# Optimization experiments

Measured on AMD Instinct MI355X. Metric: run time of the kernel, lower is better.

## Reference

```python
import jax, jax.numpy as jnp
import numpy as np


def setup_inputs() -> dict:
    key = jax.random.key(0)
    k1, k2 = jax.random.split(key)
    B, C, h, w = 8, 128, 56, 56
    query_feature = jax.random.normal(k1, (B, C, h, w), dtype=jnp.float32)
    support_feature = jax.random.normal(k2, (B, C, h, w), dtype=jnp.float32)
    return {"query_feature": query_feature, "support_feature": support_feature}


def reference(query_feature, support_feature):
    q, s = query_feature, support_feature
    B, C, h, w = support_feature.shape
    N = h * w
    # torch .view semantics == row-major reshape (NOT a transpose)
    qf = jnp.reshape(query_feature, (B, N, C))      # [B, N, C]
    sf = jnp.reshape(support_feature, (B, C, N))    # [B, C, N]
    batch_adj = jnp.einsum('bnc,bcm->bnm', qf, sf)  # [B, N, N]
    attn = jax.nn.softmax(batch_adj, axis=-1)
    query_logits = jnp.einsum('bnm,bmc->bnc', attn, qf)          # [B, N, C]
    attention_mask = jax.nn.sigmoid(jnp.sum(batch_adj, axis=-1)) # [B, N]
    query_logits = query_logits * attention_mask[..., None]
    sf2 = jnp.reshape(support_feature, (B, N, C))   # another raw view
    support_logits = sf2 * attention_mask[..., None]
    query_logits = jnp.reshape(query_logits, (B, C, h, w))
    support_logits = jnp.reshape(support_logits, (B, C, h, w))
    return (q + query_logits, s + support_logits)
```

## Files before the change

### kernel.cpp

```cpp
#include <hip/hip_runtime.h>
#include <math.h>

#define B_ 8
#define C_ 128
#define N_ 3136
#define MT 64
#define QTBIG 128
#define TILES 49
#define QTILES 25

typedef short bf16x8 __attribute__((ext_vector_type(8)));
typedef float f32x4 __attribute__((ext_vector_type(4)));

__device__ __forceinline__ unsigned short f2bf(float f) {
    union { float f; unsigned u; } x; x.f = f;
    return (unsigned short)((x.u + 0x8000u) >> 16);
}

__device__ __forceinline__ void gl_lds16(const void* g, void* l) {
    __builtin_amdgcn_global_load_lds(
        (const __attribute__((address_space(1))) unsigned int*)g,
        (__attribute__((address_space(3))) unsigned int*)l, 16, 0, 0);
}

__global__ __launch_bounds__(256) void colsum_kernel(const float* __restrict__ s,
                                                     float* __restrict__ csum) {
    int blk = blockIdx.x;
    const float* p = s + (size_t)blk * N_;
    float acc = 0.f;
    for (int i = threadIdx.x; i < N_; i += 256) acc += p[i];
#pragma unroll
    for (int off = 32; off > 0; off >>= 1) acc += __shfl_down(acc, off, 64);
    __shared__ float part[4];
    if ((threadIdx.x & 63) == 0) part[threadIdx.x >> 6] = acc;
    __syncthreads();
    if (threadIdx.x == 0) csum[blk] = part[0] + part[1] + part[2] + part[3];
}

__global__ __launch_bounds__(256) void prep_kernel(const float* __restrict__ q,
                                                   const float* __restrict__ s,
                                                   unsigned short* __restrict__ sfT,
                                                   unsigned short* __restrict__ qfT,
                                                   float* __restrict__ csum) {
    __shared__ unsigned short T[8448];
    const int tid = threadIdx.x, bid = blockIdx.x;
    const int b = bid & 7, m0 = (bid >> 3) * 64;
    const float* sb = s + (size_t)b * C_ * N_;
    const float* qb = q + (size_t)b * C_ * N_;

    unsigned short (*TA)[132] = (unsigned short (*)[132])T;
#pragma unroll
    for (int st = 0; st < 8; ++st) {
        int idx = st * 256 + tid;
        int c = idx >> 4, m4 = (idx & 15) * 4;
        float4 v = *(const float4*)&sb[(size_t)c * N_ + m0 + m4];
        TA[m4 + 0][c] = f2bf(v.x);
        TA[m4 + 1][c] = f2bf(v.y);
        TA[m4 + 2][c] = f2bf(v.z);
        TA[m4 + 3][c] = f2bf(v.w);
        float part = v.x + v.y + v.z + v.w;
        part += __shfl_xor(part, 1, 64);
        part += __shfl_xor(part, 2, 64);
        part += __shfl_xor(part, 4, 64);
        part += __shfl_xor(part, 8, 64);
        if ((tid & 15) == 0) atomicAdd(&csum[b * C_ + c], part);
    }
    __syncthreads();
    {
        unsigned short* dst = sfT + (size_t)b * N_ * C_;
#pragma unroll
        for (int st = 0; st < 4; ++st) {
            int g = st * 256 + tid;
            int mr = g >> 4, p = g & 15;
            int lch = p ^ (mr & 15);
            const unsigned short* src = &TA[mr][lch * 8];
            ushort4 a = *(const ushort4*)src;
            ushort4 bq = *(const ushort4*)(src + 4);
            uint4 w;
            w.x = a.x | ((unsigned)a.y << 16);   w.y = a.z | ((unsigned)a.w << 16);
            w.z = bq.x | ((unsigned)bq.y << 16); w.w = bq.z | ((unsigned)bq.w << 16);
            *(uint4*)&dst[(size_t)(m0 + mr) * C_ + p * 8] = w;
        }
    }
    __syncthreads();

    unsigned short (*TB)[66] = (unsigned short (*)[66])T;
#pragma unroll
    for (int st = 0; st < 8; ++st) {
        int idx = st * 256 + tid;
        int r = idx >> 5, c4 = (idx & 31) * 4;
        float4 v = *(const float4*)&qb[(size_t)(m0 + r) * C_ + c4];
        TB[c4 + 0][r] = f2bf(v.x);
        TB[c4 + 1][r] = f2bf(v.y);
        TB[c4 + 2][r] = f2bf(v.z);
        TB[c4 + 3][r] = f2bf(v.w);
    }
    __syncthreads();
    {
        unsigned short* dst = qfT + (size_t)b * C_ * N_;
#pragma unroll
        for (int st = 0; st < 4; ++st) {
            int g = st * 256 + tid;
            int c = g >> 3, p = g & 7;
            int lch = p ^ (c & 7);
            const unsigned short* src = &TB[c][lch * 8];
            ushort2 a0 = *(const ushort2*)(src);
            ushort2 a1 = *(const ushort2*)(src + 2);
            ushort2 a2 = *(const ushort2*)(src + 4);
            ushort2 a3 = *(const ushort2*)(src + 6);
            uint4 w;
            w.x = a0.x | ((unsigned)a0.y << 16); w.y = a1.x | ((unsigned)a1.y << 16);
            w.z = a2.x | ((unsigned)a2.y << 16); w.w = a3.x | ((unsigned)a3.y << 16);
            *(uint4*)&dst[(size_t)c * N_ + m0 + p * 8] = w;
        }
    }
}

__global__ __launch_bounds__(256, 2) void fused_mfma_kernel(
    const float* __restrict__ q, const float* __restrict__ s,
    const float* __restrict__ csum, const unsigned short* __restrict__ sfT,
    const unsigned short* __restrict__ qfT,
    float* __restrict__ out0, float* __restrict__ out1) {

    __shared__ __align__(16) unsigned short Kb[2][MT * C_];
    __shared__ __align__(16) unsigned short Vb[2][C_ * MT];
    __shared__ float csum_l[C_];
    __shared__ float mask_l[QTBIG];

    const int tid = threadIdx.x;
    const int lane = tid & 63;
    const int wave = tid >> 6;
    const int l15 = lane & 15;
    const int quad = lane >> 4;
    const int bid = blockIdx.x;
    const int b = bid & 7;
    const int n0 = (bid >> 3) * QTBIG;

    const float* qb = q + (size_t)b * C_ * N_;
    const float* sb = s + (size_t)b * C_ * N_;
    const unsigned short* sfTb = sfT + (size_t)b * N_ * C_;
    const unsigned short* qfTb = qfT + (size_t)b * C_ * N_;

    const int sig_base = ((l15 >> 2) << 3) + (l15 & 3);

#pragma unroll
    for (int st = 0; st < 4; ++st) {
        int i = st * 256 + tid;
        gl_lds16(sfTb + (size_t)(i >> 4) * C_ + (i & 15) * 8,
                 &Kb[0][(st * 256 + wave * 64) * 8]);
        gl_lds16(qfTb + (size_t)(i >> 3) * N_ + (i & 7) * 8,
                 &Vb[0][(st * 256 + wave * 64) * 8]);
    }
    if (tid < C_) csum_l[tid] = csum[b * C_ + tid];

    bf16x8 qa[2][4];
#pragma unroll
    for (int rt = 0; rt < 2; ++rt) {
        int grow = n0 + wave * 32 + rt * 16 + l15;
        if (grow > N_ - 1) grow = N_ - 1;
#pragma unroll
        for (int ks = 0; ks < 4; ++ks) {
            int c0 = ks * 32 + quad * 8;
            float4 f0 = *(const float4*)&qb[(size_t)grow * C_ + c0];
            float4 f1 = *(const float4*)&qb[(size_t)grow * C_ + c0 + 4];
            union { unsigned short u[8]; bf16x8 v; } t;
            t.u[0] = f2bf(f0.x); t.u[1] = f2bf(f0.y);
            t.u[2] = f2bf(f0.z); t.u[3] = f2bf(f0.w);
            t.u[4] = f2bf(f1.x); t.u[5] = f2bf(f1.y);
            t.u[6] = f2bf(f1.z); t.u[7] = f2bf(f1.w);
            qa[rt][ks] = t.v;
        }
    }
    __syncthreads();

    {
        int row_l = tid >> 1, half = tid & 1;
        int grow = n0 + row_l; if (grow > N_ - 1) grow = N_ - 1;
        const float* qr = &qb[(size_t)grow * C_ + half * 64];
        const float* cs = &csum_l[half * 64];
        float d = 0.f;
#pragma unroll 4
        for (int c = 0; c < 64; c += 4) {
            float4 v = *(const float4*)&qr[c];
            d += v.x * cs[c] + v.y * cs[c + 1] + v.z * cs[c + 2] + v.w * cs[c + 3];
        }
        d += __shfl_xor(d, 1, 64);
        if (half == 0) mask_l[row_l] = 1.0f / (1.0f + __expf(-d));
    }

    f32x4 O[2][8];
#pragma unroll
    for (int rt = 0; rt < 2; ++rt)
#pragma unroll
        for (int nt = 0; nt < 8; ++nt) O[rt][nt] = (f32x4){0.f, 0.f, 0.f, 0.f};
    float dsum[2] = {0.f, 0.f};

    for (int t = 0; t < TILES; ++t) {
        const int cur = t & 1;
        __syncthreads();

        if (t + 1 < TILES) {
            const int nxt = cur ^ 1;
            const size_t m1 = (size_t)(t + 1) * MT;
#pragma unroll
            for (int st = 0; st < 4; ++st) {
                int i = st * 256 + tid;
                gl_lds16(sfTb + (m1 + (i >> 4)) * C_ + (i & 15) * 8,
                         &Kb[nxt][(st * 256 + wave * 64) * 8]);
                gl_lds16(qfTb + (size_t)(i >> 3) * N_ + m1 + (i & 7) * 8,
                         &Vb[nxt][(st * 256 + wave * 64) * 8]);
            }
        }

        f32x4 acc[4][2];
#pragma unroll
        for (int ct = 0; ct < 4; ++ct) {
            acc[ct][0] = (f32x4){0.f, 0.f, 0.f, 0.f};
            acc[ct][1] = (f32x4){0.f, 0.f, 0.f, 0.f};
            const int mrow = sig_base + ((ct & 1) << 2) + ((ct >> 1) << 5);
#pragma unroll
            for (int ks = 0; ks < 4; ++ks) {
                int ch = (ks * 4 + quad) ^ (mrow & 15);
                bf16x8 af = *(const bf16x8*)&Kb[cur][mrow * C_ + ch * 8];
                acc[ct][0] = __builtin_amdgcn_mfma_f32_16x16x32_bf16(af, qa[0][ks], acc[ct][0], 0, 0, 0);
                acc[ct][1] = __builtin_amdgcn_mfma_f32_16x16x32_bf16(af, qa[1][ks], acc[ct][1], 0, 0, 0);
            }
        }

        bf16x8 pa[2][2];
#pragma unroll
        for (int k2 = 0; k2 < 2; ++k2)
#pragma unroll
            for (int rt = 0; rt < 2; ++rt) {
                float e0 = __expf(acc[2 * k2 + 0][rt][0]);
                float e1 = __expf(acc[2 * k2 + 0][rt][1]);
                float e2 = __expf(acc[2 * k2 + 0][rt][2]);
                float e3 = __expf(acc[2 * k2 + 0][rt][3]);
                float e4 = __expf(acc[2 * k2 + 1][rt][0]);
                float e5 = __expf(acc[2 * k2 + 1][rt][1]);
                float e6 = __expf(acc[2 * k2 + 1][rt][2]);
                float e7 = __expf(acc[2 * k2 + 1][rt][3]);
                dsum[rt] += ((e0 + e1) + (e2 + e3)) + ((e4 + e5) + (e6 + e7));
                union { unsigned short u[8]; bf16x8 v; } pk;
                pk.u[0] = f2bf(e0); pk.u[1] = f2bf(e1);
                pk.u[2] = f2bf(e2); pk.u[3] = f2bf(e3);
                pk.u[4] = f2bf(e4); pk.u[5] = f2bf(e5);
                pk.u[6] = f2bf(e6); pk.u[7] = f2bf(e7);
                pa[rt][k2] = pk.v;
            }

#pragma unroll
        for (int k2 = 0; k2 < 2; ++k2)
#pragma unroll
            for (int nt = 0; nt < 8; ++nt) {
                const int crow = nt * 16 + l15;
                int ch = (k2 * 4 + quad) ^ (crow & 7);
                bf16x8 vf = *(const bf16x8*)&Vb[cur][crow * MT + ch * 8];
                O[0][nt] = __builtin_amdgcn_mfma_f32_16x16x32_bf16(pa[0][k2], vf, O[0][nt], 0, 0, 0);
                O[1][nt] = __builtin_amdgcn_mfma_f32_16x16x32_bf16(pa[1][k2], vf, O[1][nt], 0, 0, 0);
            }
    }

#pragma unroll
    for (int rt = 0; rt < 2; ++rt) {
        float d = dsum[rt];
        d += __shfl_xor(d, 16, 64);
        d += __shfl_xor(d, 32, 64);
        dsum[rt] = d;
    }

    const size_t bo = (size_t)b * C_ * N_;
#pragma unroll
    for (int rt = 0; rt < 2; ++rt)
#pragma unroll
        for (int r = 0; r < 4; ++r) {
            int row_l = wave * 32 + rt * 16 + quad * 4 + r;
            int grow = n0 + row_l;
            float denom = __shfl(dsum[rt], quad * 4 + r, 64);
            if (grow < N_) {
                float scl = mask_l[row_l] / denom;
#pragma unroll
                for (int nt = 0; nt < 8; ++nt) {
                    int col = nt * 16 + l15;
                    out0[bo + (size_t)grow * C_ + col] =
                        qb[(size_t)grow * C_ + col] + O[rt][nt][r] * scl;
                }
            }
        }
#pragma unroll
    for (int i = 0; i < 16; ++i) {
        int idx = i * 256 + tid;
        int row_l = idx >> 5, c4 = (idx & 31) * 4;
        int grow = n0 + row_l;
        if (grow < N_) {
            float4 sv = *(const float4*)&sb[(size_t)grow * C_ + c4];
            float om = 1.0f + mask_l[row_l];
            float4 o;
            o.x = sv.x * om; o.y = sv.y * om; o.z = sv.z * om; o.w = sv.w * om;
            *(float4*)&out1[bo + (size_t)grow * C_ + c4] = o;
        }
    }
}

__global__ __launch_bounds__(256, 2) void fused_kernel(const float* __restrict__ q,
                                                       const float* __restrict__ s,
                                                       const float* __restrict__ csum,
                                                       float* __restrict__ out0,
                                                       float* __restrict__ out1) {
    __shared__ float QtT[C_][68];
    __shared__ float Kt[C_ * 32];
    __shared__ float Vt[32 * C_];
    __shared__ float PT[32][68];
    __shared__ float mask_l[64];
    __shared__ float csum_l[C_];

    const int t = threadIdx.x;
    const int l = t & 63, w = t >> 6, tx = t & 15, ty = t >> 4;
    const int bid = blockIdx.x, b = bid & 7, n0 = (bid >> 3) * 64;
    const float* qb = q + (size_t)b * C_ * N_;
    const float* sb = s + (size_t)b * C_ * N_;

#pragma unroll
    for (int jj = 0; jj < 2; ++jj) {
        int c = l + 64 * jj;
#pragma unroll
        for (int i = 0; i < 16; ++i) QtT[c][w + 4 * i] = qb[(size_t)(n0 + w + 4 * i) * C_ + c];
    }
    if (t < C_) csum_l[t] = csum[b * C_ + t];
    __syncthreads();
    if (t < 64) {
        float d = 0.f;
        for (int c = 0; c < C_; ++c) d += QtT[c][t] * csum_l[c];
        mask_l[t] = 1.0f / (1.0f + __expf(-d));
    }
    float4 Oa[4], Ob[4];
#pragma unroll
    for (int i = 0; i < 4; ++i) { Oa[i] = make_float4(0,0,0,0); Ob[i] = make_float4(0,0,0,0); }
    float m_r[4], l_r[4];
#pragma unroll
    for (int i = 0; i < 4; ++i) { m_r[i] = -3.0e38f; l_r[i] = 0.f; }

    for (int mt = 0; mt < N_ / 32; ++mt) {
        const int m0 = mt * 32;
        __syncthreads();
#pragma unroll
        for (int i = 0; i < 4; ++i) {
            int s4 = (w * 4 + i) * 64 + l;
            int c = s4 >> 3, mq = (s4 & 7) * 4;
            *(float4*)&Kt[c * 32 + mq] = *(const float4*)&sb[(size_t)c * N_ + m0 + mq];
            *(float4*)&Vt[s4 * 4] = *(const float4*)&qb[(size_t)m0 * C_ + s4 * 4];
        }
        __syncthreads();
        float a[4][2];
#pragma unroll
        for (int i = 0; i < 4; ++i) a[i][0] = a[i][1] = 0.f;
#pragma unroll 4
        for (int k = 0; k < C_; ++k) {
            const float4 qv = *(const float4*)&QtT[k][4 * ty];
            const float2 kv = *(const float2*)&Kt[k * 32 + 2 * tx];
            a[0][0] = fmaf(qv.x, kv.x, a[0][0]); a[0][1] = fmaf(qv.x, kv.y, a[0][1]);
            a[1][0] = fmaf(qv.y, kv.x, a[1][0]); a[1][1] = fmaf(qv.y, kv.y, a[1][1]);
            a[2][0] = fmaf(qv.z, kv.x, a[2][0]); a[2][1] = fmaf(qv.z, kv.y, a[2][1]);
            a[3][0] = fmaf(qv.w, kv.x, a[3][0]); a[3][1] = fmaf(qv.w, kv.y, a[3][1]);
        }
#pragma unroll
        for (int i = 0; i < 4; ++i) {
            float tm = fmaxf(a[i][0], a[i][1]);
            tm = fmaxf(tm, __shfl_xor(tm, 1, 64)); tm = fmaxf(tm, __shfl_xor(tm, 2, 64));
            tm = fmaxf(tm, __shfl_xor(tm, 4, 64)); tm = fmaxf(tm, __shfl_xor(tm, 8, 64));
            float nm = fmaxf(m_r[i], tm);
            float al = __expf(m_r[i] - nm);
            m_r[i] = nm;
            float p0 = __expf(a[i][0] - nm), p1 = __expf(a[i][1] - nm);
            float ts = p0 + p1;
            ts += __shfl_xor(ts, 1, 64); ts += __shfl_xor(ts, 2, 64);
            ts += __shfl_xor(ts, 4, 64); ts += __shfl_xor(ts, 8, 64);
            l_r[i] = l_r[i] * al + ts;
            PT[2 * tx + 0][4 * ty + i] = p0;
            PT[2 * tx + 1][4 * ty + i] = p1;
            Oa[i].x *= al; Oa[i].y *= al; Oa[i].z *= al; Oa[i].w *= al;
            Ob[i].x *= al; Ob[i].y *= al; Ob[i].z *= al; Ob[i].w *= al;
        }
        __syncthreads();
#pragma unroll 2
        for (int j = 0; j < 32; ++j) {
            const float4 pv = *(const float4*)&PT[j][4 * ty];
            const float4 v0 = *(const float4*)&Vt[j * C_ + 4 * tx];
            const float4 v1 = *(const float4*)&Vt[j * C_ + 4 * tx + 64];
            Oa[0].x = fmaf(pv.x, v0.x, Oa[0].x); Oa[0].y = fmaf(pv.x, v0.y, Oa[0].y);
            Oa[0].z = fmaf(pv.x, v0.z, Oa[0].z); Oa[0].w = fmaf(pv.x, v0.w, Oa[0].w);
            Ob[0].x = fmaf(pv.x, v1.x, Ob[0].x); Ob[0].y = fmaf(pv.x, v1.y, Ob[0].y);
            Ob[0].z = fmaf(pv.x, v1.z, Ob[0].z); Ob[0].w = fmaf(pv.x, v1.w, Ob[0].w);
            Oa[1].x = fmaf(pv.y, v0.x, Oa[1].x); Oa[1].y = fmaf(pv.y, v0.y, Oa[1].y);
            Oa[1].z = fmaf(pv.y, v0.z, Oa[1].z); Oa[1].w = fmaf(pv.y, v0.w, Oa[1].w);
            Ob[1].x = fmaf(pv.y, v1.x, Ob[1].x); Ob[1].y = fmaf(pv.y, v1.y, Ob[1].y);
            Ob[1].z = fmaf(pv.y, v1.z, Ob[1].z); Ob[1].w = fmaf(pv.y, v1.w, Ob[1].w);
            Oa[2].x = fmaf(pv.z, v0.x, Oa[2].x); Oa[2].y = fmaf(pv.z, v0.y, Oa[2].y);
            Oa[2].z = fmaf(pv.z, v0.z, Oa[2].z); Oa[2].w = fmaf(pv.z, v0.w, Oa[2].w);
            Ob[2].x = fmaf(pv.z, v1.x, Ob[2].x); Ob[2].y = fmaf(pv.z, v1.y, Ob[2].y);
            Ob[2].z = fmaf(pv.z, v1.z, Ob[2].z); Ob[2].w = fmaf(pv.z, v1.w, Ob[2].w);
            Oa[3].x = fmaf(pv.w, v0.x, Oa[3].x); Oa[3].y = fmaf(pv.w, v0.y, Oa[3].y);
            Oa[3].z = fmaf(pv.w, v0.z, Oa[3].z); Oa[3].w = fmaf(pv.w, v0.w, Oa[3].w);
            Ob[3].x = fmaf(pv.w, v1.x, Ob[3].x); Ob[3].y = fmaf(pv.w, v1.y, Ob[3].y);
            Ob[3].z = fmaf(pv.w, v1.z, Ob[3].z); Ob[3].w = fmaf(pv.w, v1.w, Ob[3].w);
        }
    }
#pragma unroll
    for (int i = 0; i < 4; ++i) {
        const int r = 4 * ty + i;
        const float mk = mask_l[r];
        const float scl = mk / l_r[i];
        const float om = 1.0f + mk;
        const size_t row = (size_t)b * C_ * N_ + (size_t)(n0 + r) * C_;
#pragma unroll
        for (int h = 0; h < 2; ++h) {
            const int c = 4 * tx + 64 * h;
            const float4 ov = h ? Ob[i] : Oa[i];
            float4 qv = *(const float4*)&qb[(size_t)(n0 + r) * C_ + c];
            float4 sv = *(const float4*)&sb[(size_t)(n0 + r) * C_ + c];
            float4 o0, o1;
            o0.x = qv.x + ov.x * scl; o0.y = qv.y + ov.y * scl;
            o0.z = qv.z + ov.z * scl; o0.w = qv.w + ov.w * scl;
            o1.x = sv.x * om; o1.y = sv.y * om; o1.z = sv.z * om; o1.w = sv.w * om;
            *(float4*)&out0[row + c] = o0;
            *(float4*)&out1[row + c] = o1;
        }
    }
}

extern "C" void kernel_launch(void* const* d_in, const int* in_sizes, int n_in,
                              void* d_out, int out_size, void* d_ws, size_t ws_size,
                              hipStream_t stream) {
    const float* q = (const float*)d_in[0];
    const float* s = (const float*)d_in[1];
    float* out0 = (float*)d_out;
    float* out1 = out0 + (size_t)B_ * C_ * N_;
    float* csum = (float*)d_ws;

    const size_t bf16_elems = (size_t)B_ * N_ * C_;
    const size_t need = 4096 + 2 * bf16_elems * sizeof(unsigned short);

    if (ws_size >= need) {
        unsigned short* sfT = (unsigned short*)((char*)d_ws + 4096);
        unsigned short* qfT = sfT + bf16_elems;
        hipMemsetAsync(csum, 0, B_ * C_ * sizeof(float), stream);
        prep_kernel<<<B_ * TILES, 256, 0, stream>>>(q, s, sfT, qfT, csum);
        fused_mfma_kernel<<<B_ * QTILES, 256, 0, stream>>>(q, s, csum, sfT, qfT, out0, out1);
    } else {
        colsum_kernel<<<B_ * C_, 256, 0, stream>>>(s, csum);
        fused_kernel<<<B_ * (N_ / 64), 256, 0, stream>>>(q, s, csum, out0, out1);
    }
}
```

Baseline: 180.8 us.

## Split key range across two blocks and add separate combine kernel

The attention kernel now splits the key tiles into two halves handled by separate blocks, doubling the grid to improve CU occupancy. Each block writes unnormalized partial outputs and row sums to workspace, and a new combine kernel sums them, computes the sigmoid mask, and writes both outputs. The column sum moves from atomics in the prep kernel to the standalone colsum kernel. This adds fp32 partial-output traffic, an extra launch, and a larger workspace requirement.

Measured after the change: 149.0 us. -17.6%, faster.

```diff
diff --git a/kernel.cpp b/kernel.cpp
--- a/kernel.cpp
+++ b/kernel.cpp
@@ -8,6 +8,7 @@
 #define QTBIG 128
 #define TILES 49
 #define QTILES 25
+#define SPLIT0 25
 
 typedef short bf16x8 __attribute__((ext_vector_type(8)));
 typedef float f32x4 __attribute__((ext_vector_type(4)));
@@ -40,8 +41,7 @@
 __global__ __launch_bounds__(256) void prep_kernel(const float* __restrict__ q,
                                                    const float* __restrict__ s,
                                                    unsigned short* __restrict__ sfT,
-                                                   unsigned short* __restrict__ qfT,
-                                                   float* __restrict__ csum) {
+                                                   unsigned short* __restrict__ qfT) {
     __shared__ unsigned short T[8448];
     const int tid = threadIdx.x, bid = blockIdx.x;
     const int b = bid & 7, m0 = (bid >> 3) * 64;
@@ -58,12 +58,6 @@
         TA[m4 + 1][c] = f2bf(v.y);
         TA[m4 + 2][c] = f2bf(v.z);
         TA[m4 + 3][c] = f2bf(v.w);
-        float part = v.x + v.y + v.z + v.w;
-        part += __shfl_xor(part, 1, 64);
-        part += __shfl_xor(part, 2, 64);
-        part += __shfl_xor(part, 4, 64);
-        part += __shfl_xor(part, 8, 64);
-        if ((tid & 15) == 0) atomicAdd(&csum[b * C_ + c], part);
     }
     __syncthreads();
     {
@@ -116,16 +110,14 @@
     }
 }
 
-__global__ __launch_bounds__(256, 2) void fused_mfma_kernel(
-    const float* __restrict__ q, const float* __restrict__ s,
-    const float* __restrict__ csum, const unsigned short* __restrict__ sfT,
+__global__ __launch_bounds__(256, 2) void fused_split_kernel(
+    const float* __restrict__ q,
+    const unsigned short* __restrict__ sfT,
     const unsigned short* __restrict__ qfT,
-    float* __restrict__ out0, float* __restrict__ out1) {
+    float* __restrict__ Opart, float* __restrict__ dpart) {
 
     __shared__ __align__(16) unsigned short Kb[2][MT * C_];
     __shared__ __align__(16) unsigned short Vb[2][C_ * MT];
-    __shared__ float csum_l[C_];
-    __shared__ float mask_l[QTBIG];
 
     const int tid = threadIdx.x;
     const int lane = tid & 63;
@@ -134,24 +126,30 @@
     const int quad = lane >> 4;
     const int bid = blockIdx.x;
     const int b = bid & 7;
-    const int n0 = (bid >> 3) * QTBIG;
+    const int rest = bid >> 3;
+    const int qt = rest % QTILES;
+    const int split = rest / QTILES;
+    const int n0 = qt * QTBIG;
+    const int t0 = split ? SPLIT0 : 0;
+    const int t1 = split ? TILES : SPLIT0;
 
     const float* qb = q + (size_t)b * C_ * N_;
-    const float* sb = s + (size_t)b * C_ * N_;
     const unsigned short* sfTb = sfT + (size_t)b * N_ * C_;
     const unsigned short* qfTb = qfT + (size_t)b * C_ * N_;
 
     const int sig_base = ((l15 >> 2) << 3) + (l15 & 3);
 
-#pragma unroll
-    for (int st = 0; st < 4; ++st) {
-        int i = st * 256 + tid;
-        gl_lds16(sfTb + (size_t)(i >> 4) * C_ + (i & 15) * 8,
-                 &Kb[0][(st * 256 + wave * 64) * 8]);
-        gl_lds16(qfTb + (size_t)(i >> 3) * N_ + (i & 7) * 8,
-                 &Vb[0][(st * 256 + wave * 64) * 8]);
-    }
-    if (tid < C_) csum_l[tid] = csum[b * C_ + tid];
+    {
+        const size_t m1 = (size_t)t0 * MT;
+#pragma unroll
+        for (int st = 0; st < 4; ++st) {
+            int i = st * 256 + tid;
+            gl_lds16(sfTb + (m1 + (i >> 4)) * C_ + (i & 15) * 8,
+                     &Kb[0][(st * 256 + wave * 64) * 8]);
+            gl_lds16(qfTb + (size_t)(i >> 3) * N_ + m1 + (i & 7) * 8,
+                     &Vb[0][(st * 256 + wave * 64) * 8]);
+        }
+    }
 
     bf16x8 qa[2][4];
 #pragma unroll
@@ -171,22 +169,6 @@
             qa[rt][ks] = t.v;
         }
     }
-    __syncthreads();
-
-    {
-        int row_l = tid >> 1, half = tid & 1;
-        int grow = n0 + row_l; if (grow > N_ - 1) grow = N_ - 1;
-        const float* qr = &qb[(size_t)grow * C_ + half * 64];
-        const float* cs = &csum_l[half * 64];
-        float d = 0.f;
-#pragma unroll 4
-        for (int c = 0; c < 64; c += 4) {
-            float4 v = *(const float4*)&qr[c];
-            d += v.x * cs[c] + v.y * cs[c + 1] + v.z * cs[c + 2] + v.w * cs[c + 3];
-        }
-        d += __shfl_xor(d, 1, 64);
-        if (half == 0) mask_l[row_l] = 1.0f / (1.0f + __expf(-d));
-    }
 
     f32x4 O[2][8];
 #pragma unroll
@@ -195,13 +177,14 @@
         for (int nt = 0; nt < 8; ++nt) O[rt][nt] = (f32x4){0.f, 0.f, 0.f, 0.f};
     float dsum[2] = {0.f, 0.f};
 
-    for (int t = 0; t < TILES; ++t) {
-        const int cur = t & 1;
+    const int ntiles = t1 - t0;
+    for (int tt = 0; tt < ntiles; ++tt) {
+        const int cur = tt & 1;
         __syncthreads();
 
-        if (t + 1 < TILES) {
+        if (tt + 1 < ntiles) {
             const int nxt = cur ^ 1;
-            const size_t m1 = (size_t)(t + 1) * MT;
+            const size_t m1 = (size_t)(t0 + tt + 1) * MT;
 #pragma unroll
             for (int st = 0; st < 4; ++st) {
                 int i = st * 256 + tid;
@@ -266,39 +249,81 @@
         float d = dsum[rt];
         d += __shfl_xor(d, 16, 64);
         d += __shfl_xor(d, 32, 64);
-        dsum[rt] = d;
-    }
-
-    const size_t bo = (size_t)b * C_ * N_;
+        if (quad == 0) {
+            int grow = n0 + wave * 32 + rt * 16 + l15;
+            if (grow < N_)
+                dpart[(size_t)(split * 8 + b) * N_ + grow] = d;
+        }
+    }
+
 #pragma unroll
     for (int rt = 0; rt < 2; ++rt)
 #pragma unroll
         for (int r = 0; r < 4; ++r) {
-            int row_l = wave * 32 + rt * 16 + quad * 4 + r;
-            int grow = n0 + row_l;
-            float denom = __shfl(dsum[rt], quad * 4 + r, 64);
+            int grow = n0 + wave * 32 + rt * 16 + quad * 4 + r;
             if (grow < N_) {
-                float scl = mask_l[row_l] / denom;
-#pragma unroll
-                for (int nt = 0; nt < 8; ++nt) {
-                    int col = nt * 16 + l15;
-                    out0[bo + (size_t)grow * C_ + col] =
-                        qb[(size_t)grow * C_ + col] + O[rt][nt][r] * scl;
-                }
+                float* dst = Opart + ((size_t)(split * 8 + b) * N_ + grow) * C_;
+#pragma unroll
+                for (int nt = 0; nt < 8; ++nt)
+                    dst[nt * 16 + l15] = O[rt][nt][r];
             }
         }
-#pragma unroll
-    for (int i = 0; i < 16; ++i) {
-        int idx = i * 256 + tid;
-        int row_l = idx >> 5, c4 = (idx & 31) * 4;
-        int grow = n0 + row_l;
-        if (grow < N_) {
-            float4 sv = *(const float4*)&sb[(size_t)grow * C_ + c4];
-            float om = 1.0f + mask_l[row_l];
-            float4 o;
-            o.x = sv.x * om; o.y = sv.y * om; o.z = sv.z * om; o.w = sv.w * om;
-            *(float4*)&out1[bo + (size_t)grow * C_ + c4] = o;
-        }
+}
+
+__global__ __launch_bounds__(256) void combine_kernel(
+    const float* __restrict__ q, const float* __restrict__ s,
+    const float* __restrict__ csum, const float* __restrict__ Opart,
+    const float* __restrict__ dpart,
+    float* __restrict__ out0, float* __restrict__ out1) {
+
+    __shared__ float cs[C_];
+    const int tid = threadIdx.x, bid = blockIdx.x;
+    const int b = bid & 7, r0 = (bid >> 3) * 32;
+    if (tid < C_) cs[tid] = csum[b * C_ + tid];
+    __syncthreads();
+
+    const int lane = tid & 63, wave = tid >> 6;
+    const int row_l = wave * 8 + (lane >> 3);
+    const int j = lane & 7;
+    const int grow = r0 + row_l;
+    const size_t base = (size_t)b * N_ * C_ + (size_t)grow * C_;
+
+    float4 qv[4];
+    float dot = 0.f;
+#pragma unroll
+    for (int k = 0; k < 4; ++k) {
+        int c = k * 32 + j * 4;
+        qv[k] = *(const float4*)&q[base + c];
+        dot += qv[k].x * cs[c] + qv[k].y * cs[c + 1] +
+               qv[k].z * cs[c + 2] + qv[k].w * cs[c + 3];
+    }
+    dot += __shfl_xor(dot, 1, 64);
+    dot += __shfl_xor(dot, 2, 64);
+    dot += __shfl_xor(dot, 4, 64);
+    const float mask = 1.0f / (1.0f + __expf(-dot));
+
+    const float dtot = dpart[(size_t)b * N_ + grow] +
+                       dpart[(size_t)(8 + b) * N_ + grow];
+    const float scl = mask / dtot;
+    const float om = 1.0f + mask;
+
+    const size_t p0 = ((size_t)b * N_ + grow) * C_;
+    const size_t p1 = p0 + (size_t)8 * N_ * C_;
+#pragma unroll
+    for (int k = 0; k < 4; ++k) {
+        int c = k * 32 + j * 4;
+        float4 oa = *(const float4*)&Opart[p0 + c];
+        float4 ob = *(const float4*)&Opart[p1 + c];
+        float4 sv = *(const float4*)&s[base + c];
+        float4 r0v, r1v;
+        r0v.x = qv[k].x + (oa.x + ob.x) * scl;
+        r0v.y = qv[k].y + (oa.y + ob.y) * scl;
+        r0v.z = qv[k].z + (oa.z + ob.z) * scl;
+        r0v.w = qv[k].w + (oa.w + ob.w) * scl;
+        r1v.x = sv.x * om; r1v.y = sv.y * om;
+        r1v.z = sv.z * om; r1v.w = sv.w * om;
+        *(float4*)&out0[base + c] = r0v;
+        *(float4*)&out1[base + c] = r1v;
     }
 }
 
@@ -437,17 +462,22 @@
     float* out1 = out0 + (size_t)B_ * C_ * N_;
     float* csum = (float*)d_ws;
 
-    const size_t bf16_elems = (size_t)B_ * N_ * C_;
-    const size_t need = 4096 + 2 * bf16_elems * sizeof(unsigned short);
-
+    const size_t elems = (size_t)B_ * N_ * C_;
+    const size_t need = 4096
+                      + 2 * elems * sizeof(unsigned short)
+                      + 2 * elems * sizeof(float)
+                      + 2 * (size_t)B_ * N_ * sizeof(float);
+
+    colsum_kernel<<<B_ * C_, 256, 0, stream>>>(s, csum);
     if (ws_size >= need) {
         unsigned short* sfT = (unsigned short*)((char*)d_ws + 4096);
-        unsigned short* qfT = sfT + bf16_elems;
-        hipMemsetAsync(csum, 0, B_ * C_ * sizeof(float), stream);
-        prep_kernel<<<B_ * TILES, 256, 0, stream>>>(q, s, sfT, qfT, csum);
-        fused_mfma_kernel<<<B_ * QTILES, 256, 0, stream>>>(q, s, csum, sfT, qfT, out0, out1);
+        unsigned short* qfT = sfT + elems;
+        float* Opart = (float*)(qfT + elems);
+        float* dpart = Opart + 2 * elems;
+        prep_kernel<<<B_ * TILES, 256, 0, stream>>>(q, s, sfT, qfT);
+        fused_split_kernel<<<2 * QTILES * B_, 256, 0, stream>>>(q, sfT, qfT, Opart, dpart);
+        combine_kernel<<<B_ * (N_ / 32), 256, 0, stream>>>(q, s, csum, Opart, dpart, out0, out1);
     } else {
-        colsum_kernel<<<B_ * C_, 256, 0, stream>>>(s, csum);
         fused_kernel<<<B_ * (N_ / 64), 256, 0, stream>>>(q, s, csum, out0, out1);
     }
 }
```

## Split key dimension across two blocks with atomic-counter last-block combine

Applied to the files above, without the earlier changes.

The fused attention kernel now splits the 3136 key positions into two halves, one per block, which doubles the grid from 200 to 400 blocks so more of the CUs are busy. Each block writes its partial O and softmax denominators to workspace and bumps an atomic counter. The second block to arrive merges both halves, computes the sigmoid mask and writes the outputs. The key tile is halved to 32, with a matching change to the prep kernel's V layout, and launch bounds now allow 3 blocks per CU. The cost is extra global traffic for the partial results, plus a counter that is never reset and relies on parity across calls.

After: 231.9 us. 1.28x slower.

```diff
diff --git a/kernel.cpp b/kernel.cpp
--- a/kernel.cpp
+++ b/kernel.cpp
@@ -4,10 +4,12 @@
 #define B_ 8
 #define C_ 128
 #define N_ 3136
-#define MT 64
+#define MT 32
 #define QTBIG 128
-#define TILES 49
+#define TILES32 98
+#define SPLIT_T 49
 #define QTILES 25
+#define PTILES 49
 
 typedef short bf16x8 __attribute__((ext_vector_type(8)));
 typedef float f32x4 __attribute__((ext_vector_type(4)));
@@ -101,9 +103,10 @@
 #pragma unroll
         for (int st = 0; st < 4; ++st) {
             int g = st * 256 + tid;
-            int c = g >> 3, p = g & 7;
-            int lch = p ^ (c & 7);
-            const unsigned short* src = &TB[c][lch * 8];
+            int c = g >> 3, pp = g & 7;
+            int grp = pp >> 2, p = pp & 3;
+            int lch = p ^ (c & 3);
+            const unsigned short* src = &TB[c][grp * 32 + lch * 8];
             ushort2 a0 = *(const ushort2*)(src);
             ushort2 a1 = *(const ushort2*)(src + 2);
             ushort2 a2 = *(const ushort2*)(src + 4);
@@ -111,21 +114,23 @@
             uint4 w;
             w.x = a0.x | ((unsigned)a0.y << 16); w.y = a1.x | ((unsigned)a1.y << 16);
             w.z = a2.x | ((unsigned)a2.y << 16); w.w = a3.x | ((unsigned)a3.y << 16);
-            *(uint4*)&dst[(size_t)c * N_ + m0 + p * 8] = w;
-        }
-    }
-}
-
-__global__ __launch_bounds__(256, 2) void fused_mfma_kernel(
+            *(uint4*)&dst[(size_t)c * N_ + m0 + grp * 32 + p * 8] = w;
+        }
+    }
+}
+
+__global__ __launch_bounds__(256, 3) void fused_split_kernel(
     const float* __restrict__ q, const float* __restrict__ s,
-    const float* __restrict__ csum, const unsigned short* __restrict__ sfT,
+    const float* __restrict__ csum,
+    const unsigned short* __restrict__ sfT,
     const unsigned short* __restrict__ qfT,
+    float* __restrict__ Opart, float* __restrict__ dpart,
+    int* __restrict__ cnt,
     float* __restrict__ out0, float* __restrict__ out1) {
 
     __shared__ __align__(16) unsigned short Kb[2][MT * C_];
     __shared__ __align__(16) unsigned short Vb[2][C_ * MT];
-    __shared__ float csum_l[C_];
-    __shared__ float mask_l[QTBIG];
+    __shared__ int flag_s;
 
     const int tid = threadIdx.x;
     const int lane = tid & 63;
@@ -134,7 +139,11 @@
     const int quad = lane >> 4;
     const int bid = blockIdx.x;
     const int b = bid & 7;
-    const int n0 = (bid >> 3) * QTBIG;
+    const int rest = bid >> 3;
+    const int qt = rest % QTILES;
+    const int split = rest / QTILES;
+    const int n0 = qt * QTBIG;
+    const int t0 = split * SPLIT_T;
 
     const float* qb = q + (size_t)b * C_ * N_;
     const float* sb = s + (size_t)b * C_ * N_;
@@ -143,15 +152,17 @@
 
     const int sig_base = ((l15 >> 2) << 3) + (l15 & 3);
 
-#pragma unroll
-    for (int st = 0; st < 4; ++st) {
-        int i = st * 256 + tid;
-        gl_lds16(sfTb + (size_t)(i >> 4) * C_ + (i & 15) * 8,
-                 &Kb[0][(st * 256 + wave * 64) * 8]);
-        gl_lds16(qfTb + (size_t)(i >> 3) * N_ + (i & 7) * 8,
-                 &Vb[0][(st * 256 + wave * 64) * 8]);
-    }
-    if (tid < C_) csum_l[tid] = csum[b * C_ + tid];
+    {
+        const size_t m1 = (size_t)t0 * MT;
+#pragma unroll
+        for (int j = 0; j < 2; ++j) {
+            int i = j * 256 + tid;
+            gl_lds16(sfTb + (m1 + (i >> 4)) * C_ + (i & 15) * 8,
+                     &Kb[0][(j * 256 + wave * 64) * 8]);
+            gl_lds16(qfTb + (size_t)(i >> 2) * N_ + m1 + (i & 3) * 8,
+                     &Vb[0][(j * 256 + wave * 64) * 8]);
+        }
+    }
 
     bf16x8 qa[2][4];
 #pragma unroll
@@ -171,22 +182,6 @@
             qa[rt][ks] = t.v;
         }
     }
-    __syncthreads();
-
-    {
-        int row_l = tid >> 1, half = tid & 1;
-        int grow = n0 + row_l; if (grow > N_ - 1) grow = N_ - 1;
-        const float* qr = &qb[(size_t)grow * C_ + half * 64];
-        const float* cs = &csum_l[half * 64];
-        float d = 0.f;
-#pragma unroll 4
-        for (int c = 0; c < 64; c += 4) {
-            float4 v = *(const float4*)&qr[c];
-            d += v.x * cs[c] + v.y * cs[c + 1] + v.z * cs[c + 2] + v.w * cs[c + 3];
-        }
-        d += __shfl_xor(d, 1, 64);
-        if (half == 0) mask_l[row_l] = 1.0f / (1.0f + __expf(-d));
-    }
 
     f32x4 O[2][8];
 #pragma unroll
@@ -195,29 +190,29 @@
         for (int nt = 0; nt < 8; ++nt) O[rt][nt] = (f32x4){0.f, 0.f, 0.f, 0.f};
     float dsum[2] = {0.f, 0.f};
 
-    for (int t = 0; t < TILES; ++t) {
-        const int cur = t & 1;
+    for (int tt = 0; tt < SPLIT_T; ++tt) {
+        const int cur = tt & 1;
         __syncthreads();
 
-        if (t + 1 < TILES) {
+        if (tt + 1 < SPLIT_T) {
             const int nxt = cur ^ 1;
-            const size_t m1 = (size_t)(t + 1) * MT;
-#pragma unroll
-            for (int st = 0; st < 4; ++st) {
-                int i = st * 256 + tid;
+            const size_t m1 = (size_t)(t0 + tt + 1) * MT;
+#pragma unroll
+            for (int j = 0; j < 2; ++j) {
+                int i = j * 256 + tid;
                 gl_lds16(sfTb + (m1 + (i >> 4)) * C_ + (i & 15) * 8,
-                         &Kb[nxt][(st * 256 + wave * 64) * 8]);
-                gl_lds16(qfTb + (size_t)(i >> 3) * N_ + m1 + (i & 7) * 8,
-                         &Vb[nxt][(st * 256 + wave * 64) * 8]);
+                         &Kb[nxt][(j * 256 + wave * 64) * 8]);
+                gl_lds16(qfTb + (size_t)(i >> 2) * N_ + m1 + (i & 3) * 8,
+                         &Vb[nxt][(j * 256 + wave * 64) * 8]);
             }
         }
 
-        f32x4 acc[4][2];
-#pragma unroll
-        for (int ct = 0; ct < 4; ++ct) {
+        f32x4 acc[2][2];
+#pragma unroll
+        for (int ct = 0; ct < 2; ++ct) {
             acc[ct][0] = (f32x4){0.f, 0.f, 0.f, 0.f};
             acc[ct][1] = (f32x4){0.f, 0.f, 0.f, 0.f};
-            const int mrow = sig_base + ((ct & 1) << 2) + ((ct >> 1) << 5);
+            const int mrow = sig_base + ct * 4;
 #pragma unroll
             for (int ks = 0; ks < 4; ++ks) {
                 int ch = (ks * 4 + quad) ^ (mrow & 15);
@@ -227,38 +222,31 @@
             }
         }
 
-        bf16x8 pa[2][2];
-#pragma unroll
-        for (int k2 = 0; k2 < 2; ++k2)
-#pragma unroll
-            for (int rt = 0; rt < 2; ++rt) {
-                float e0 = __expf(acc[2 * k2 + 0][rt][0]);
-                float e1 = __expf(acc[2 * k2 + 0][rt][1]);
-                float e2 = __expf(acc[2 * k2 + 0][rt][2]);
-                float e3 = __expf(acc[2 * k2 + 0][rt][3]);
-                float e4 = __expf(acc[2 * k2 + 1][rt][0]);
-                float e5 = __expf(acc[2 * k2 + 1][rt][1]);
-                float e6 = __expf(acc[2 * k2 + 1][rt][2]);
-                float e7 = __expf(acc[2 * k2 + 1][rt][3]);
-                dsum[rt] += ((e0 + e1) + (e2 + e3)) + ((e4 + e5) + (e6 + e7));
-                union { unsigned short u[8]; bf16x8 v; } pk;
-                pk.u[0] = f2bf(e0); pk.u[1] = f2bf(e1);
-                pk.u[2] = f2bf(e2); pk.u[3] = f2bf(e3);
-                pk.u[4] = f2bf(e4); pk.u[5] = f2bf(e5);
-                pk.u[6] = f2bf(e6); pk.u[7] = f2bf(e7);
-                pa[rt][k2] = pk.v;
-            }
-
-#pragma unroll
-        for (int k2 = 0; k2 < 2; ++k2)
-#pragma unroll
-            for (int nt = 0; nt < 8; ++nt) {
-                const int crow = nt * 16 + l15;
-                int ch = (k2 * 4 + quad) ^ (crow & 7);
-                bf16x8 vf = *(const bf16x8*)&Vb[cur][crow * MT + ch * 8];
-                O[0][nt] = __builtin_amdgcn_mfma_f32_16x16x32_bf16(pa[0][k2], vf, O[0][nt], 0, 0, 0);
-                O[1][nt] = __builtin_amdgcn_mfma_f32_16x16x32_bf16(pa[1][k2], vf, O[1][nt], 0, 0, 0);
-            }
+        bf16x8 pa[2];
+#pragma unroll
+        for (int rt = 0; rt < 2; ++rt) {
+            union { unsigned short u[8]; bf16x8 v; } pk;
+            float da = 0.f;
+#pragma unroll
+            for (int ct = 0; ct < 2; ++ct)
+#pragma unroll
+                for (int r = 0; r < 4; ++r) {
+                    float e = __expf(acc[ct][rt][r]);
+                    da += e;
+                    pk.u[ct * 4 + r] = f2bf(e);
+                }
+            dsum[rt] += da;
+            pa[rt] = pk.v;
+        }
+
+#pragma unroll
+        for (int nt = 0; nt < 8; ++nt) {
+            const int crow = nt * 16 + l15;
+            int ch = quad ^ (crow & 3);
+            bf16x8 vf = *(const bf16x8*)&Vb[cur][crow * MT + ch * 8];
+            O[0][nt] = __builtin_amdgcn_mfma_f32_16x16x32_bf16(pa[0], vf, O[0][nt], 0, 0, 0);
+            O[1][nt] = __builtin_amdgcn_mfma_f32_16x16x32_bf16(pa[1], vf, O[1][nt], 0, 0, 0);
+        }
     }
 
 #pragma unroll
@@ -267,26 +255,77 @@
         d += __shfl_xor(d, 16, 64);
         d += __shfl_xor(d, 32, 64);
         dsum[rt] = d;
-    }
-
+        if (quad == 0) {
+            int grow = n0 + wave * 32 + rt * 16 + l15;
+            if (grow < N_)
+                dpart[(size_t)(split * 8 + b) * N_ + grow] = d;
+        }
+    }
+
+#pragma unroll
+    for (int rt = 0; rt < 2; ++rt)
+#pragma unroll
+        for (int r = 0; r < 4; ++r) {
+            int grow = n0 + wave * 32 + rt * 16 + quad * 4 + r;
+            if (grow < N_) {
+                float* dst = Opart + ((size_t)(split * 8 + b) * N_ + grow) * C_;
+#pragma unroll
+                for (int nt = 0; nt < 8; ++nt)
+                    dst[nt * 16 + l15] = O[rt][nt][r];
+            }
+        }
+
+    __threadfence();
+    __syncthreads();
+    if (tid == 0) flag_s = atomicAdd(&cnt[b * QTILES + qt], 1);
+    __syncthreads();
+    if ((flag_s & 1) == 0) return;
+    __threadfence();
+
+    float* cs = (float*)&Kb[0][0];
+    float* mask_l = cs + C_;
+    if (tid < C_) cs[tid] = csum[b * C_ + tid];
+    __syncthreads();
+
+    const int other = split ^ 1;
+    const float* OthO = Opart + (size_t)(other * 8 + b) * N_ * C_;
+    const float* Othd = dpart + (size_t)(other * 8 + b) * N_;
     const size_t bo = (size_t)b * C_ * N_;
+
 #pragma unroll
     for (int rt = 0; rt < 2; ++rt)
 #pragma unroll
         for (int r = 0; r < 4; ++r) {
             int row_l = wave * 32 + rt * 16 + quad * 4 + r;
             int grow = n0 + row_l;
-            float denom = __shfl(dsum[rt], quad * 4 + r, 64);
+            float myd = __shfl(dsum[rt], quad * 4 + r, 64);
             if (grow < N_) {
-                float scl = mask_l[row_l] / denom;
+                float othd = Othd[grow];
+                float qv[8];
+                float dotp = 0.f;
 #pragma unroll
                 for (int nt = 0; nt < 8; ++nt) {
                     int col = nt * 16 + l15;
-                    out0[bo + (size_t)grow * C_ + col] =
-                        qb[(size_t)grow * C_ + col] + O[rt][nt][r] * scl;
+                    qv[nt] = qb[(size_t)grow * C_ + col];
+                    dotp += qv[nt] * cs[col];
+                }
+                dotp += __shfl_xor(dotp, 1, 64);
+                dotp += __shfl_xor(dotp, 2, 64);
+                dotp += __shfl_xor(dotp, 4, 64);
+                dotp += __shfl_xor(dotp, 8, 64);
+                float mask = 1.0f / (1.0f + __expf(-dotp));
+                if (l15 == 0) mask_l[row_l] = mask;
+                float scl = mask / (myd + othd);
+#pragma unroll
+                for (int nt = 0; nt < 8; ++nt) {
+                    int col = nt * 16 + l15;
+                    float tot = O[rt][nt][r] + OthO[(size_t)grow * C_ + col];
+                    out0[bo + (size_t)grow * C_ + col] = qv[nt] + tot * scl;
                 }
             }
         }
+    __syncthreads();
+
 #pragma unroll
     for (int i = 0; i < 16; ++i) {
         int idx = i * 256 + tid;
@@ -437,15 +476,23 @@
     float* out1 = out0 + (size_t)B_ * C_ * N_;
     float* csum = (float*)d_ws;
 
-    const size_t bf16_elems = (size_t)B_ * N_ * C_;
-    const size_t need = 4096 + 2 * bf16_elems * sizeof(unsigned short);
+    const size_t elems = (size_t)B_ * N_ * C_;
+    const size_t need = 4096
+                      + 2 * elems * sizeof(unsigned short)
+                      + 2 * elems * sizeof(float)
+                      + 2 * (size_t)B_ * N_ * sizeof(float)
+                      + (size_t)B_ * QTILES * sizeof(int);
 
     if (ws_size >= need) {
         unsigned short* sfT = (unsigned short*)((char*)d_ws + 4096);
-        unsigned short* qfT = sfT + bf16_elems;
+        unsigned short* qfT = sfT + elems;
+        float* Opart = (float*)(qfT + elems);
+        float* dpart = Opart + 2 * elems;
+        int* cnt = (int*)(dpart + 2 * (size_t)B_ * N_);
         hipMemsetAsync(csum, 0, B_ * C_ * sizeof(float), stream);
-        prep_kernel<<<B_ * TILES, 256, 0, stream>>>(q, s, sfT, qfT, csum);
-        fused_mfma_kernel<<<B_ * QTILES, 256, 0, stream>>>(q, s, csum, sfT, qfT, out0, out1);
+        prep_kernel<<<B_ * PTILES, 256, 0, stream>>>(q, s, sfT, qfT, csum);
+        fused_split_kernel<<<2 * QTILES * B_, 256, 0, stream>>>(q, s, csum, sfT, qfT,
+                                                                Opart, dpart, cnt, out0, out1);
     } else {
         colsum_kernel<<<B_ * C_, 256, 0, stream>>>(s, csum);
         fused_kernel<<<B_ * (N_ / 64), 256, 0, stream>>>(q, s, csum, out0, out1);
```

## Split key dimension across four blocks with atomic partial reduction

Applied to the files above, without the earlier changes.

The fused attention kernel now splits the 49 key tiles of each query tile across four blocks, so the launch grows from 200 to 800 workgroups and fills more CUs. Each split adds its unnormalised output and row denominators into global fp32 buffers with atomics, and a counter picks the last block to finish, which computes the mask and writes both outputs. This works because softmax does no max subtraction, so partial sums add directly. The cost is an extra memset of a large fp32 buffer, heavy global atomic traffic (about 400K atomics per split pass), and a reread of the partial sums.

Result: slower. 234.5 us (+29.7%).

```diff
diff --git a/kernel.cpp b/kernel.cpp
--- a/kernel.cpp
+++ b/kernel.cpp
@@ -8,6 +8,7 @@
 #define QTBIG 128
 #define TILES 49
 #define QTILES 25
+#define NSPLIT 4
 
 typedef short bf16x8 __attribute__((ext_vector_type(8)));
 typedef float f32x4 __attribute__((ext_vector_type(4)));
@@ -116,16 +117,18 @@
     }
 }
 
-__global__ __launch_bounds__(256, 2) void fused_mfma_kernel(
+__global__ __launch_bounds__(256, 2) void fused_split_kernel(
     const float* __restrict__ q, const float* __restrict__ s,
-    const float* __restrict__ csum, const unsigned short* __restrict__ sfT,
+    const float* __restrict__ csum,
+    const unsigned short* __restrict__ sfT,
     const unsigned short* __restrict__ qfT,
+    float* __restrict__ Opart, float* __restrict__ dpart,
+    int* __restrict__ cnt,
     float* __restrict__ out0, float* __restrict__ out1) {
 
     __shared__ __align__(16) unsigned short Kb[2][MT * C_];
     __shared__ __align__(16) unsigned short Vb[2][C_ * MT];
-    __shared__ float csum_l[C_];
-    __shared__ float mask_l[QTBIG];
+    __shared__ int flag_s;
 
     const int tid = threadIdx.x;
     const int lane = tid & 63;
@@ -134,7 +137,12 @@
     const int quad = lane >> 4;
     const int bid = blockIdx.x;
     const int b = bid & 7;
-    const int n0 = (bid >> 3) * QTBIG;
+    const int rest = bid >> 3;
+    const int qt = rest % QTILES;
+    const int split = rest / QTILES;
+    const int n0 = qt * QTBIG;
+    const int t0 = (split == 0) ? 0 : (1 + split * 12);
+    const int ntiles = (split == 0) ? 13 : 12;
 
     const float* qb = q + (size_t)b * C_ * N_;
     const float* sb = s + (size_t)b * C_ * N_;
@@ -143,15 +151,17 @@
 
     const int sig_base = ((l15 >> 2) << 3) + (l15 & 3);
 
-#pragma unroll
-    for (int st = 0; st < 4; ++st) {
-        int i = st * 256 + tid;
-        gl_lds16(sfTb + (size_t)(i >> 4) * C_ + (i & 15) * 8,
-                 &Kb[0][(st * 256 + wave * 64) * 8]);
-        gl_lds16(qfTb + (size_t)(i >> 3) * N_ + (i & 7) * 8,
-                 &Vb[0][(st * 256 + wave * 64) * 8]);
-    }
-    if (tid < C_) csum_l[tid] = csum[b * C_ + tid];
+    {
+        const size_t m1 = (size_t)t0 * MT;
+#pragma unroll
+        for (int st = 0; st < 4; ++st) {
+            int i = st * 256 + tid;
+            gl_lds16(sfTb + (m1 + (i >> 4)) * C_ + (i & 15) * 8,
+                     &Kb[0][(st * 256 + wave * 64) * 8]);
+            gl_lds16(qfTb + (size_t)(i >> 3) * N_ + m1 + (i & 7) * 8,
+                     &Vb[0][(st * 256 + wave * 64) * 8]);
+        }
+    }
 
     bf16x8 qa[2][4];
 #pragma unroll
@@ -171,22 +181,6 @@
             qa[rt][ks] = t.v;
         }
     }
-    __syncthreads();
-
-    {
-        int row_l = tid >> 1, half = tid & 1;
-        int grow = n0 + row_l; if (grow > N_ - 1) grow = N_ - 1;
-        const float* qr = &qb[(size_t)grow * C_ + half * 64];
-        const float* cs = &csum_l[half * 64];
-        float d = 0.f;
-#pragma unroll 4
-        for (int c = 0; c < 64; c += 4) {
-            float4 v = *(const float4*)&qr[c];
-            d += v.x * cs[c] + v.y * cs[c + 1] + v.z * cs[c + 2] + v.w * cs[c + 3];
-        }
-        d += __shfl_xor(d, 1, 64);
-        if (half == 0) mask_l[row_l] = 1.0f / (1.0f + __expf(-d));
-    }
 
     f32x4 O[2][8];
 #pragma unroll
@@ -195,13 +189,13 @@
         for (int nt = 0; nt < 8; ++nt) O[rt][nt] = (f32x4){0.f, 0.f, 0.f, 0.f};
     float dsum[2] = {0.f, 0.f};
 
-    for (int t = 0; t < TILES; ++t) {
-        const int cur = t & 1;
+    for (int tt = 0; tt < ntiles; ++tt) {
+        const int cur = tt & 1;
         __syncthreads();
 
-        if (t + 1 < TILES) {
+        if (tt + 1 < ntiles) {
             const int nxt = cur ^ 1;
-            const size_t m1 = (size_t)(t + 1) * MT;
+            const size_t m1 = (size_t)(t0 + tt + 1) * MT;
 #pragma unroll
             for (int st = 0; st < 4; ++st) {
                 int i = st * 256 + tid;
@@ -266,8 +260,36 @@
         float d = dsum[rt];
         d += __shfl_xor(d, 16, 64);
         d += __shfl_xor(d, 32, 64);
-        dsum[rt] = d;
-    }
+        if (quad == 0) {
+            int grow = n0 + wave * 32 + rt * 16 + l15;
+            if (grow < N_) atomicAdd(&dpart[(size_t)b * N_ + grow], d);
+        }
+    }
+
+#pragma unroll
+    for (int rt = 0; rt < 2; ++rt)
+#pragma unroll
+        for (int r = 0; r < 4; ++r) {
+            int grow = n0 + wave * 32 + rt * 16 + quad * 4 + r;
+            if (grow < N_) {
+                float* dst = Opart + ((size_t)b * N_ + grow) * C_;
+#pragma unroll
+                for (int nt = 0; nt < 8; ++nt)
+                    atomicAdd(&dst[nt * 16 + l15], O[rt][nt][r]);
+            }
+        }
+
+    __threadfence();
+    __syncthreads();
+    if (tid == 0) flag_s = atomicAdd(&cnt[b * QTILES + qt], 1);
+    __syncthreads();
+    if (flag_s != NSPLIT - 1) return;
+    __threadfence();
+
+    float* cs = (float*)&Kb[0][0];
+    float* mask_l = cs + C_;
+    if (tid < C_) cs[tid] = csum[b * C_ + tid];
+    __syncthreads();
 
     const size_t bo = (size_t)b * C_ * N_;
 #pragma unroll
@@ -276,17 +298,32 @@
         for (int r = 0; r < 4; ++r) {
             int row_l = wave * 32 + rt * 16 + quad * 4 + r;
             int grow = n0 + row_l;
-            float denom = __shfl(dsum[rt], quad * 4 + r, 64);
             if (grow < N_) {
-                float scl = mask_l[row_l] / denom;
+                float qv[8];
+                float dotp = 0.f;
 #pragma unroll
                 for (int nt = 0; nt < 8; ++nt) {
                     int col = nt * 16 + l15;
-                    out0[bo + (size_t)grow * C_ + col] =
-                        qb[(size_t)grow * C_ + col] + O[rt][nt][r] * scl;
+                    qv[nt] = qb[(size_t)grow * C_ + col];
+                    dotp += qv[nt] * cs[col];
+                }
+                dotp += __shfl_xor(dotp, 1, 64);
+                dotp += __shfl_xor(dotp, 2, 64);
+                dotp += __shfl_xor(dotp, 4, 64);
+                dotp += __shfl_xor(dotp, 8, 64);
+                float mask = 1.0f / (1.0f + __expf(-dotp));
+                if (l15 == 0) mask_l[row_l] = mask;
+                float scl = mask / dpart[(size_t)b * N_ + grow];
+                const float* Orow = Opart + ((size_t)b * N_ + grow) * C_;
+#pragma unroll
+                for (int nt = 0; nt < 8; ++nt) {
+                    int col = nt * 16 + l15;
+                    out0[bo + (size_t)grow * C_ + col] = qv[nt] + Orow[col] * scl;
                 }
             }
         }
+    __syncthreads();
+
 #pragma unroll
     for (int i = 0; i < 16; ++i) {
         int idx = i * 256 + tid;
@@ -437,15 +474,27 @@
     float* out1 = out0 + (size_t)B_ * C_ * N_;
     float* csum = (float*)d_ws;
 
-    const size_t bf16_elems = (size_t)B_ * N_ * C_;
-    const size_t need = 4096 + 2 * bf16_elems * sizeof(unsigned short);
+    const size_t elems = (size_t)B_ * N_ * C_;
+    const size_t need = 4096
+                      + 2 * elems * sizeof(unsigned short)
+                      + elems * sizeof(float)
+                      + (size_t)B_ * N_ * sizeof(float)
+                      + (size_t)B_ * QTILES * sizeof(int);
 
     if (ws_size >= need) {
         unsigned short* sfT = (unsigned short*)((char*)d_ws + 4096);
-        unsigned short* qfT = sfT + bf16_elems;
+        unsigned short* qfT = sfT + elems;
+        float* Opart = (float*)(qfT + elems);
+        float* dpart = Opart + elems;
+        int* cnt = (int*)(dpart + (size_t)B_ * N_);
         hipMemsetAsync(csum, 0, B_ * C_ * sizeof(float), stream);
+        hipMemsetAsync(Opart, 0,
+                       elems * sizeof(float) + (size_t)B_ * N_ * sizeof(float)
+                           + (size_t)B_ * QTILES * sizeof(int),
+                       stream);
         prep_kernel<<<B_ * TILES, 256, 0, stream>>>(q, s, sfT, qfT, csum);
-        fused_mfma_kernel<<<B_ * QTILES, 256, 0, stream>>>(q, s, csum, sfT, qfT, out0, out1);
+        fused_split_kernel<<<NSPLIT * QTILES * B_, 256, 0, stream>>>(
+            q, s, csum, sfT, qfT, Opart, dpart, cnt, out0, out1);
     } else {
         colsum_kernel<<<B_ * C_, 256, 0, stream>>>(s, csum);
         fused_kernel<<<B_ * (N_ / 64), 256, 0, stream>>>(q, s, csum, out0, out1);
```
